# Optimization experiments

Hardware: AMD Instinct MI355X
Metric: run time of the kernel (lower is better)

Reference implementation:

```python
import jax, jax.numpy as jnp
import numpy as np
import math

D_MODEL = 512
N_HEADS = 8
WINDOW = 5
B, S = 4, 2048


def setup_inputs() -> dict:
    key = jax.random.key(0)
    ks = jax.random.split(key, 16)
    d = D_MODEL

    def lin(k, fan_in, fan_out):
        bound = 1.0 / math.sqrt(fan_in)
        kw, kb = jax.random.split(k)
        W = jax.random.uniform(kw, (fan_in, fan_out), jnp.float32, -bound, bound)
        b = jax.random.uniform(kb, (fan_out,), jnp.float32, -bound, bound)
        return W, b

    x = jax.random.normal(ks[0], (B, S, d), jnp.float32)
    W1, b1 = lin(ks[1], d, 2 * d)      # mapping layer 1
    W2, b2 = lin(ks[2], 2 * d, d)      # mapping layer 2
    Wq, bq = lin(ks[3], d, d)
    Wk, bk = lin(ks[4], d, d)
    Wv, bv = lin(ks[5], d, d)
    Wo, bo = lin(ks[6], d, d)
    return dict(x=x, W1=W1, b1=b1, W2=W2, b2=b2, Wq=Wq, bq=bq,
                Wk=Wk, bk=bk, Wv=Wv, bv=bv, Wo=Wo, bo=bo)


def reference(x, W1, b1, W2, b2, Wq, bq, Wk, bk, Wv, bv, Wo, bo):
    Bsz, S_, d = x.shape
    h = N_HEADS
    hd = d // h

    # mapping MLP: Linear -> ReLU -> Linear
    xm = jax.nn.relu(x @ W1 + b1) @ W2 + b2

    def split_heads(t):  # [B,S,d] -> [B,h,S,hd]
        return t.reshape(Bsz, S_, h, hd).transpose(0, 2, 1, 3)

    Q = split_heads(xm @ Wq + bq)
    K = split_heads(xm @ Wk + bk)
    V = split_heads(xm @ Wv + bv)

    scores = jnp.einsum('bhqd,bhkd->bhqk', Q, K) / math.sqrt(hd)

    # inverse sliding-window mask: positions with |i-j| <= window are EXCLUDED
    idx = jnp.arange(S_)
    adjacent = jnp.abs(idx[:, None] - idx[None, :]) <= WINDOW  # [S,S] bool
    scores = jnp.where(adjacent[None, None], -1e9, scores)

    attn = jax.nn.softmax(scores, axis=-1)
    out = jnp.einsum('bhqk,bhkd->bhqd', attn, V)
    out = out.transpose(0, 2, 1, 3).reshape(Bsz, S_, d)
    return out @ Wo + bo
```

## Files before the change

### kernel.cpp

```cpp
#include <hip/hip_runtime.h>
#include <stdint.h>

typedef __attribute__((ext_vector_type(8))) short bf16x8;
typedef __attribute__((ext_vector_type(4))) float f32x4;

__device__ __forceinline__ float bf2f(uint16_t u) {
    union { uint32_t u; float f; } c; c.u = ((uint32_t)u) << 16; return c.f;
}
__device__ __forceinline__ uint16_t f2bf(float f) {
    union { float f; uint32_t u; } c; c.f = f;
    uint32_t r = c.u + 0x7fffu + ((c.u >> 16) & 1u);
    return (uint16_t)(r >> 16);
}
__device__ __forceinline__ uint32_t pk2bf(float a, float b) {
#if __has_builtin(__builtin_amdgcn_cvt_pk_bf16_f32)
    auto v = __builtin_amdgcn_cvt_pk_bf16_f32(a, b);
    uint32_t u; __builtin_memcpy(&u, &v, 4); return u;
#else
    return (uint32_t)f2bf(a) | ((uint32_t)f2bf(b) << 16);
#endif
}
__device__ __forceinline__ float fexp2(float x) {
#if __has_builtin(__builtin_amdgcn_exp2f)
    return __builtin_amdgcn_exp2f(x);
#else
    return exp2f(x);
#endif
}

__device__ __forceinline__ void gld_lds16(const uint16_t* g, uint16_t* l) {
    __builtin_amdgcn_global_load_lds(
        (const __attribute__((address_space(1))) void*)g,
        (__attribute__((address_space(3))) void*)l, 16, 0, 0);
}

__global__ void prep_all(const float* __restrict__ x,
                         const float* __restrict__ W1, const float* __restrict__ W2,
                         const float* __restrict__ Wq, const float* __restrict__ Wk,
                         const float* __restrict__ Wv, const float* __restrict__ Wo,
                         const float* __restrict__ b1, const float* __restrict__ b2,
                         const float* __restrict__ bq, const float* __restrict__ bk,
                         const float* __restrict__ bv, const float* __restrict__ bo,
                         uint16_t* __restrict__ W1T, uint16_t* __restrict__ W2T,
                         uint16_t* __restrict__ WqkvT, uint16_t* __restrict__ WoT,
                         uint16_t* __restrict__ xb, uint16_t* __restrict__ bbase)
{
    const int id = blockIdx.x;
    const int tx = threadIdx.x, ty = threadIdx.y;
    const int tid = ty * 32 + tx;
    if (id < 2048) {
        __shared__ uint16_t t[32][33];
        const float* src; uint16_t* dst; int R, C, tile;
        if      (id < 512)  { src = W1; dst = W1T;              R = 512;  C = 1024; tile = id; }
        else if (id < 1024) { src = W2; dst = W2T;              R = 1024; C = 512;  tile = id - 512; }
        else if (id < 1280) { src = Wq; dst = WqkvT;            R = 512;  C = 512;  tile = id - 1024; }
        else if (id < 1536) { src = Wk; dst = WqkvT + 512*512;  R = 512;  C = 512;  tile = id - 1280; }
        else if (id < 1792) { src = Wv; dst = WqkvT + 1024*512; R = 512;  C = 512;  tile = id - 1536; }
        else                { src = Wo; dst = WoT;              R = 512;  C = 512;  tile = id - 1792; }
        const int ntx = C / 32;
        const int bx = (tile % ntx) * 32, by = (tile / ntx) * 32;
#pragma unroll
        for (int i = ty; i < 32; i += 8) t[i][tx] = f2bf(src[(size_t)(by + i) * C + bx + tx]);
        __syncthreads();
#pragma unroll
        for (int i = ty; i < 32; i += 8) dst[(size_t)(bx + i) * R + by + tx] = t[tx][i];
    } else if (id < 6144) {
        int i = (id - 2048) * 256 + tid;
        float4 v = ((const float4*)x)[i];
        ushort4 o;
        o.x = f2bf(v.x); o.y = f2bf(v.y); o.z = f2bf(v.z); o.w = f2bf(v.w);
        ((ushort4*)xb)[i] = o;
    } else {
        int i = (id - 6144) * 256 + tid;
        if      (i < 1024) bbase[i] = f2bf(b1[i]);
        else if (i < 1536) bbase[i] = f2bf(b2[i - 1024]);
        else if (i < 2048) bbase[i] = f2bf(bq[i - 1536]);
        else if (i < 2560) bbase[i] = f2bf(bk[i - 2048]);
        else if (i < 3072) bbase[i] = f2bf(bv[i - 2560]);
        else if (i < 3584) bbase[i] = f2bf(bo[i - 3072]);
    }
}

template<int RELU, int F32OUT>
__global__ __launch_bounds__(256)
void gemm_k(const uint16_t* __restrict__ A, const uint16_t* __restrict__ Bt,
            const uint16_t* __restrict__ bias, void* __restrict__ Cv,
            int M, int N, int K)
{
    __shared__ __align__(16) uint16_t lsA[128 * 64];
    __shared__ __align__(16) uint16_t lsB[128 * 64];

    const int tid = threadIdx.x, lane = tid & 63;
    const int wid = tid >> 6;
    const int quad = lane >> 4, lm = lane & 15;
    const int wm = wid >> 1, wn = wid & 1;
    const int m0 = blockIdx.y * 128, n0 = blockIdx.x * 128;

    f32x4 acc[4][4];
#pragma unroll
    for (int i = 0; i < 4; ++i)
#pragma unroll
        for (int j = 0; j < 4; ++j) acc[i][j] = (f32x4){0.f, 0.f, 0.f, 0.f};

    for (int k0 = 0; k0 < K; k0 += 64) {
        __syncthreads();
#pragma unroll
        for (int c4 = 0; c4 < 4; ++c4) {
            const int chunk = c4 * 256 + tid;
            const int r = chunk >> 3, lc = (chunk & 7) ^ (r & 7);
            gld_lds16(A  + (size_t)(m0 + r) * K + k0 + lc * 8, lsA + (size_t)chunk * 8);
            gld_lds16(Bt + (size_t)(n0 + r) * K + k0 + lc * 8, lsB + (size_t)chunk * 8);
        }
        __syncthreads();

#pragma unroll
        for (int kh = 0; kh < 2; ++kh) {
            bf16x8 af[4], bfr[4];
#pragma unroll
            for (int t = 0; t < 4; ++t) {
                const int pcA = ((kh * 4 + quad) ^ (lm & 7));
                af[t]  = *(const bf16x8*)(lsA + (wm * 64 + t * 16 + lm) * 64 + pcA * 8);
                bfr[t] = *(const bf16x8*)(lsB + (wn * 64 + t * 16 + lm) * 64 + pcA * 8);
            }
#pragma unroll
            for (int i = 0; i < 4; ++i)
#pragma unroll
                for (int j = 0; j < 4; ++j)
                    acc[i][j] = __builtin_amdgcn_mfma_f32_16x16x32_bf16(af[i], bfr[j], acc[i][j], 0, 0, 0);
        }
    }

#pragma unroll
    for (int i = 0; i < 4; ++i) {
        const int r0 = m0 + wm * 64 + i * 16 + quad * 4;
#pragma unroll
        for (int j = 0; j < 4; ++j) {
            const int col = n0 + wn * 64 + j * 16 + lm;
            const float bvj = bf2f(bias[col]);
#pragma unroll
            for (int r = 0; r < 4; ++r) {
                float v = acc[i][j][r] + bvj;
                if (RELU) v = fmaxf(v, 0.f);
                if (F32OUT) ((float*)Cv)[(size_t)(r0 + r) * N + col] = v;
                else        ((uint16_t*)Cv)[(size_t)(r0 + r) * N + col] = f2bf(v);
            }
        }
    }
}

template<int RELU, int F32OUT>
__global__ __launch_bounds__(256)
void gemm_k64(const uint16_t* __restrict__ A, const uint16_t* __restrict__ Bt,
              const uint16_t* __restrict__ bias, void* __restrict__ Cv,
              int M, int N, int K)
{
    __shared__ __align__(16) uint16_t lsA[64 * 64];
    __shared__ __align__(16) uint16_t lsB[128 * 64];

    const int tid = threadIdx.x, lane = tid & 63;
    const int wid = tid >> 6;
    const int quad = lane >> 4, lm = lane & 15;
    const int wm = wid >> 1, wn = wid & 1;
    const int m0 = blockIdx.y * 64, n0 = blockIdx.x * 128;

    f32x4 acc[2][4];
#pragma unroll
    for (int i = 0; i < 2; ++i)
#pragma unroll
        for (int j = 0; j < 4; ++j) acc[i][j] = (f32x4){0.f, 0.f, 0.f, 0.f};

    for (int k0 = 0; k0 < K; k0 += 64) {
        __syncthreads();
#pragma unroll
        for (int c4 = 0; c4 < 2; ++c4) {
            const int chunk = c4 * 256 + tid;
            const int r = chunk >> 3, lc = (chunk & 7) ^ (r & 7);
            gld_lds16(A + (size_t)(m0 + r) * K + k0 + lc * 8, lsA + (size_t)chunk * 8);
        }
#pragma unroll
        for (int c4 = 0; c4 < 4; ++c4) {
            const int chunk = c4 * 256 + tid;
            const int r = chunk >> 3, lc = (chunk & 7) ^ (r & 7);
            gld_lds16(Bt + (size_t)(n0 + r) * K + k0 + lc * 8, lsB + (size_t)chunk * 8);
        }
        __syncthreads();

#pragma unroll
        for (int kh = 0; kh < 2; ++kh) {
            const int pc = ((kh * 4 + quad) ^ (lm & 7));
            bf16x8 af[2], bfr[4];
#pragma unroll
            for (int t = 0; t < 2; ++t)
                af[t] = *(const bf16x8*)(lsA + (wm * 32 + t * 16 + lm) * 64 + pc * 8);
#pragma unroll
            for (int t = 0; t < 4; ++t)
                bfr[t] = *(const bf16x8*)(lsB + (wn * 64 + t * 16 + lm) * 64 + pc * 8);
#pragma unroll
            for (int i = 0; i < 2; ++i)
#pragma unroll
                for (int j = 0; j < 4; ++j)
                    acc[i][j] = __builtin_amdgcn_mfma_f32_16x16x32_bf16(af[i], bfr[j], acc[i][j], 0, 0, 0);
        }
    }

#pragma unroll
    for (int i = 0; i < 2; ++i) {
        const int r0 = m0 + wm * 32 + i * 16 + quad * 4;
#pragma unroll
        for (int j = 0; j < 4; ++j) {
            const int col = n0 + wn * 64 + j * 16 + lm;
            const float bvj = bf2f(bias[col]);
#pragma unroll
            for (int r = 0; r < 4; ++r) {
                float v = acc[i][j][r] + bvj;
                if (RELU) v = fmaxf(v, 0.f);
                if (F32OUT) ((float*)Cv)[(size_t)(r0 + r) * N + col] = v;
                else        ((uint16_t*)Cv)[(size_t)(r0 + r) * N + col] = f2bf(v);
            }
        }
    }
}

__global__ __launch_bounds__(256)
void gemm_qkv_s(const uint16_t* __restrict__ A, const uint16_t* __restrict__ Bt,
                const uint16_t* __restrict__ bq, const uint16_t* __restrict__ bk,
                const uint16_t* __restrict__ bv_,
                uint16_t* __restrict__ qk, uint16_t* __restrict__ Vt)
{
    __shared__ __align__(16) uint16_t lsA[128 * 64];
    __shared__ __align__(16) uint16_t lsB[128 * 64];

    const int tid = threadIdx.x, lane = tid & 63;
    const int wid = tid >> 6;
    const int quad = lane >> 4, lm = lane & 15;
    const int wm = wid >> 1, wn = wid & 1;
    const int m0 = blockIdx.y * 128, n0 = blockIdx.x * 128;
    const int part = n0 >> 9;
    const uint16_t* B = (part == 0) ? bq : (part == 1) ? bk : bv_;
    const int K = 512;

    f32x4 acc[4][4];
#pragma unroll
    for (int i = 0; i < 4; ++i)
#pragma unroll
        for (int j = 0; j < 4; ++j) acc[i][j] = (f32x4){0.f, 0.f, 0.f, 0.f};

    for (int k0 = 0; k0 < K; k0 += 64) {
        __syncthreads();
#pragma unroll
        for (int c4 = 0; c4 < 4; ++c4) {
            const int chunk = c4 * 256 + tid;
            const int r = chunk >> 3, lc = (chunk & 7) ^ (r & 7);
            gld_lds16(A  + (size_t)(m0 + r) * K + k0 + lc * 8, lsA + (size_t)chunk * 8);
            gld_lds16(Bt + (size_t)(n0 + r) * K + k0 + lc * 8, lsB + (size_t)chunk * 8);
        }
        __syncthreads();

#pragma unroll
        for (int kh = 0; kh < 2; ++kh) {
            const int pc = ((kh * 4 + quad) ^ (lm & 7));
            bf16x8 af[4], bfr[4];
#pragma unroll
            for (int t = 0; t < 4; ++t) {
                af[t]  = *(const bf16x8*)(lsA + (wm * 64 + t * 16 + lm) * 64 + pc * 8);
                bfr[t] = *(const bf16x8*)(lsB + (wn * 64 + t * 16 + lm) * 64 + pc * 8);
            }
#pragma unroll
            for (int i = 0; i < 4; ++i)
#pragma unroll
                for (int j = 0; j < 4; ++j)
                    acc[i][j] = __builtin_amdgcn_mfma_f32_16x16x32_bf16(af[i], bfr[j], acc[i][j], 0, 0, 0);
        }
    }

#pragma unroll
    for (int i = 0; i < 4; ++i) {
        const int mb = m0 + wm * 64 + i * 16 + quad * 4;
#pragma unroll
        for (int j = 0; j < 4; ++j) {
            const int nl = (n0 & 511) + wn * 64 + j * 16 + lm;
            const float bvj = bf2f(B[nl]);
            if (part < 2) {
#pragma unroll
                for (int r = 0; r < 4; ++r)
                    qk[(size_t)(mb + r) * 1024 + part * 512 + nl] = f2bf(acc[i][j][r] + bvj);
            } else {
                const int h = nl >> 6, d = nl & 63;
                const int b = mb >> 11, s0 = mb & 2047;
                const int sp = (s0 & ~31) | ((s0 & 12) << 1) | (((s0 >> 4) & 1) << 2);
                const size_t base = ((size_t)(((b << 3) | h)) * 64 + d) * 2048 + sp;
#pragma unroll
                for (int r = 0; r < 4; ++r)
                    Vt[base + r] = f2bf(acc[i][j][r] + bvj);
            }
        }
    }
}

__global__ __launch_bounds__(256, 2)
void attn_k(const uint16_t* __restrict__ qk, const uint16_t* __restrict__ Vt,
            uint16_t* __restrict__ Out)
{
    __shared__ __align__(16) uint16_t lsK[2][128 * 64];
    __shared__ __align__(16) uint16_t lsV[2][64 * 128];

    const int tid = threadIdx.x, lane = tid & 63, wid = tid >> 6;
    const int quad = lane >> 4, lm = lane & 15;
    const int bh = blockIdx.y, b = bh >> 3, h = bh & 7;
    const int q0 = blockIdx.x * 128;
    const float cscale = 0.125f * 1.44269504088896f;

    bf16x8 qf[2][2];
#pragma unroll
    for (int i = 0; i < 2; ++i)
#pragma unroll
        for (int ks = 0; ks < 2; ++ks) {
            bf16x8 q = *(const bf16x8*)(qk +
                (size_t)(b * 2048 + q0 + wid * 32 + i * 16 + lm) * 1024 + h * 64 + ks * 32 + quad * 8);
#pragma unroll
            for (int e = 0; e < 8; ++e)
                q[e] = (short)f2bf(bf2f((uint16_t)q[e]) * cscale);
            qf[i][ks] = q;
        }

    f32x4 oacc[2][4];
#pragma unroll
    for (int i = 0; i < 2; ++i)
#pragma unroll
        for (int n = 0; n < 4; ++n) oacc[i][n] = (f32x4){0.f, 0.f, 0.f, 0.f};
    float lrow[2] = {0.f, 0.f};

    auto stage = [&](int j0, int bb) {
#pragma unroll
        for (int c4 = 0; c4 < 4; ++c4) {
            const int chunk = c4 * 256 + tid;
            const int r = chunk >> 3, lc = (chunk & 7) ^ (r & 7);
            gld_lds16(qk + (size_t)(b * 2048 + j0 + r) * 1024 + 512 + h * 64 + lc * 8,
                      &lsK[bb][(size_t)chunk * 8]);
        }
#pragma unroll
        for (int c4 = 0; c4 < 4; ++c4) {
            const int chunk = c4 * 256 + tid;
            const int d = chunk >> 4, lc = (chunk & 15) ^ (d & 15);
            gld_lds16(Vt + (size_t)(bh * 64 + d) * 2048 + j0 + lc * 8,
                      &lsV[bb][(size_t)chunk * 8]);
        }
    };

    auto compute = [&](int j0, int bb) {
        const uint16_t* Kb = &lsK[bb][0];
        const uint16_t* Vb = &lsV[bb][0];

        f32x4 sacc[2][8];
#pragma unroll
        for (int i = 0; i < 2; ++i)
#pragma unroll
            for (int j = 0; j < 8; ++j) sacc[i][j] = (f32x4){0.f, 0.f, 0.f, 0.f};
        __builtin_amdgcn_s_setprio(1);
#pragma unroll
        for (int ks = 0; ks < 2; ++ks)
#pragma unroll
            for (int j = 0; j < 8; ++j) {
                const int pc = (ks * 4 + quad) ^ (lm & 7);
                bf16x8 kf = *(const bf16x8*)(Kb + (j * 16 + lm) * 64 + pc * 8);
#pragma unroll
                for (int i = 0; i < 2; ++i)
                    sacc[i][j] = __builtin_amdgcn_mfma_f32_16x16x32_bf16(kf, qf[i][ks], sacc[i][j], 0, 0, 0);
            }
        __builtin_amdgcn_s_setprio(0);

        if ((j0 + 127 >= q0 - 5) && (j0 <= q0 + 127 + 5)) {
#pragma unroll
            for (int i = 0; i < 2; ++i) {
                const int qr = q0 + wid * 32 + i * 16 + lm;
#pragma unroll
                for (int j = 0; j < 8; ++j)
#pragma unroll
                    for (int r = 0; r < 4; ++r) {
                        int kc = j0 + j * 16 + quad * 4 + r;
                        int dd = qr - kc; if (dd < 0) dd = -dd;
                        if (dd <= 5) sacc[i][j][r] = -1e30f;
                    }
            }
        }

#pragma unroll
        for (int ks = 0; ks < 4; ++ks) {
            bf16x8 pa[2];
#pragma unroll
            for (int i = 0; i < 2; ++i) {
                const float p0 = fexp2(sacc[i][2 * ks + 0][0]);
                const float p1 = fexp2(sacc[i][2 * ks + 0][1]);
                const float p2 = fexp2(sacc[i][2 * ks + 0][2]);
                const float p3 = fexp2(sacc[i][2 * ks + 0][3]);
                const float p4 = fexp2(sacc[i][2 * ks + 1][0]);
                const float p5 = fexp2(sacc[i][2 * ks + 1][1]);
                const float p6 = fexp2(sacc[i][2 * ks + 1][2]);
                const float p7 = fexp2(sacc[i][2 * ks + 1][3]);
                lrow[i] += ((p0 + p1) + (p2 + p3)) + ((p4 + p5) + (p6 + p7));
                union { bf16x8 v; uint32_t u[4]; } c;
                c.u[0] = pk2bf(p0, p1);
                c.u[1] = pk2bf(p2, p3);
                c.u[2] = pk2bf(p4, p5);
                c.u[3] = pk2bf(p6, p7);
                pa[i] = c.v;
            }
            __builtin_amdgcn_s_setprio(1);
#pragma unroll
            for (int n = 0; n < 4; ++n) {
                const int pc = (ks * 4 + quad) ^ lm;
                bf16x8 vf = *(const bf16x8*)(Vb + (n * 16 + lm) * 128 + pc * 8);
#pragma unroll
                for (int i = 0; i < 2; ++i)
                    oacc[i][n] = __builtin_amdgcn_mfma_f32_16x16x32_bf16(pa[i], vf, oacc[i][n], 0, 0, 0);
            }
            __builtin_amdgcn_s_setprio(0);
        }
    };

    stage(0, 0);
    int cur = 0;
#pragma unroll 1
    for (int jt = 0; jt < 15; ++jt) {
        stage((jt + 1) * 128, cur ^ 1);
        asm volatile("s_waitcnt vmcnt(8)" ::: "memory");
        __builtin_amdgcn_sched_barrier(0);
        __builtin_amdgcn_s_barrier();
        compute(jt * 128, cur);
        __builtin_amdgcn_s_barrier();
        cur ^= 1;
    }
    asm volatile("s_waitcnt vmcnt(0)" ::: "memory");
    __builtin_amdgcn_sched_barrier(0);
    __builtin_amdgcn_s_barrier();
    compute(15 * 128, cur);

#pragma unroll
    for (int i = 0; i < 2; ++i) {
        float l = lrow[i];
        l += __shfl_xor(l, 16);
        l += __shfl_xor(l, 32);
        const float inv = 1.f / (l + 1e-30f);
#pragma unroll
        for (int r = 0; r < 4; ++r) {
            const float invr = __shfl(inv, quad * 4 + r, 16);
            const int s = q0 + wid * 32 + i * 16 + quad * 4 + r;
#pragma unroll
            for (int n = 0; n < 4; ++n)
                Out[(size_t)(b * 2048 + s) * 512 + h * 64 + n * 16 + lm] = f2bf(oacc[i][n][r] * invr);
        }
    }
}

extern "C" void kernel_launch(void* const* d_in, const int* in_sizes, int n_in,
                              void* d_out, int out_size, void* d_ws, size_t ws_size,
                              hipStream_t stream)
{
    const float* x  = (const float*)d_in[0];
    const float* W1 = (const float*)d_in[1];
    const float* b1 = (const float*)d_in[2];
    const float* W2 = (const float*)d_in[3];
    const float* b2 = (const float*)d_in[4];
    const float* Wq = (const float*)d_in[5];
    const float* bq = (const float*)d_in[6];
    const float* Wk = (const float*)d_in[7];
    const float* bk = (const float*)d_in[8];
    const float* Wv = (const float*)d_in[9];
    const float* bv = (const float*)d_in[10];
    const float* Wo = (const float*)d_in[11];
    const float* bo = (const float*)d_in[12];
    (void)in_sizes; (void)n_in; (void)out_size; (void)ws_size;

    char* ws = (char*)d_ws;
    const size_t MiB = 1024 * 1024;
    uint16_t* xb    = (uint16_t*)(ws + 0);
    uint16_t* W1T   = (uint16_t*)(ws + 8 * MiB);
    uint16_t* W2T   = (uint16_t*)(ws + 9 * MiB);
    uint16_t* WqkvT = (uint16_t*)(ws + 10 * MiB);
    uint16_t* WoT   = (uint16_t*)(ws + 11 * MiB + 512 * 1024);
    uint16_t* bbase = (uint16_t*)(ws + 12 * MiB);
    uint16_t* b1b = bbase, *b2b = bbase + 1024, *bqb = bbase + 1536;
    uint16_t* bkb = bbase + 2048, *bvb = bbase + 2560, *bob = bbase + 3072;
    uint16_t* xm1   = (uint16_t*)(ws + 13 * MiB);
    uint16_t* xm    = (uint16_t*)(ws + 29 * MiB);
    uint16_t* qk    = xm1;
    uint16_t* att   = xm;
    uint16_t* Vt    = xb;

    prep_all<<<6158, dim3(32, 8), 0, stream>>>(x, W1, W2, Wq, Wk, Wv, Wo,
                                               b1, b2, bq, bk, bv, bo,
                                               W1T, W2T, WqkvT, WoT, xb, bbase);

    gemm_k<1,0>  <<<dim3(8, 64),  256, 0, stream>>>(xb,  W1T, b1b, xm1, 8192, 1024, 512);
    gemm_k64<0,0><<<dim3(4, 128), 256, 0, stream>>>(xm1, W2T, b2b, xm,  8192, 512, 1024);
    gemm_qkv_s   <<<dim3(12, 64), 256, 0, stream>>>(xm, WqkvT, bqb, bkb, bvb, qk, Vt);
    attn_k       <<<dim3(16, 32), 256, 0, stream>>>(qk, Vt, att);
    gemm_k64<0,1><<<dim3(4, 128), 256, 0, stream>>>(att, WoT, bob, d_out, 8192, 512, 512);
}
```

Measured before the change: 217.2 us.

## Split attention key tile across two wave groups with LDS reduction

Doubles the attention block to 512 threads. Two groups of four waves each handle half of every 128-key tile for the same 128 queries. Their partial PV accumulators and row sums are then combined through LDS before normalisation. The aim is more waves in flight and fewer registers per wave, to hide latency in the attention loop. The cost is an extra LDS reduction, extra barriers, and duplicated Q fragment loads.

```diff
diff --git a/kernel.cpp b/kernel.cpp
--- a/kernel.cpp
+++ b/kernel.cpp
@@ -297,14 +297,14 @@
     }
 }
 
-__global__ __launch_bounds__(256, 2)
+__global__ __launch_bounds__(512, 4)
 void attn_k(const uint16_t* __restrict__ qk, const uint16_t* __restrict__ Vt,
             uint16_t* __restrict__ Out)
 {
-    __shared__ __align__(16) uint16_t lsK[2][128 * 64];
-    __shared__ __align__(16) uint16_t lsV[2][64 * 128];
+    __shared__ __align__(16) uint16_t lsAll[2][16384];
 
     const int tid = threadIdx.x, lane = tid & 63, wid = tid >> 6;
+    const int qw = wid & 3, kh2 = wid >> 2;
     const int quad = lane >> 4, lm = lane & 15;
     const int bh = blockIdx.y, b = bh >> 3, h = bh & 7;
     const int q0 = blockIdx.x * 128;
@@ -316,7 +316,7 @@
 #pragma unroll
         for (int ks = 0; ks < 2; ++ks) {
             bf16x8 q = *(const bf16x8*)(qk +
-                (size_t)(b * 2048 + q0 + wid * 32 + i * 16 + lm) * 1024 + h * 64 + ks * 32 + quad * 8);
+                (size_t)(b * 2048 + q0 + qw * 32 + i * 16 + lm) * 1024 + h * 64 + ks * 32 + quad * 8);
 #pragma unroll
             for (int e = 0; e < 8; ++e)
                 q[e] = (short)f2bf(bf2f((uint16_t)q[e]) * cscale);
@@ -331,38 +331,40 @@
     float lrow[2] = {0.f, 0.f};
 
     auto stage = [&](int j0, int bb) {
-#pragma unroll
-        for (int c4 = 0; c4 < 4; ++c4) {
-            const int chunk = c4 * 256 + tid;
+        uint16_t* lsK = &lsAll[bb][0];
+        uint16_t* lsV = &lsAll[bb][8192];
+#pragma unroll
+        for (int c2 = 0; c2 < 2; ++c2) {
+            const int chunk = c2 * 512 + tid;
             const int r = chunk >> 3, lc = (chunk & 7) ^ (r & 7);
             gld_lds16(qk + (size_t)(b * 2048 + j0 + r) * 1024 + 512 + h * 64 + lc * 8,
-                      &lsK[bb][(size_t)chunk * 8]);
-        }
-#pragma unroll
-        for (int c4 = 0; c4 < 4; ++c4) {
-            const int chunk = c4 * 256 + tid;
+                      lsK + (size_t)chunk * 8);
+        }
+#pragma unroll
+        for (int c2 = 0; c2 < 2; ++c2) {
+            const int chunk = c2 * 512 + tid;
             const int d = chunk >> 4, lc = (chunk & 15) ^ (d & 15);
             gld_lds16(Vt + (size_t)(bh * 64 + d) * 2048 + j0 + lc * 8,
-                      &lsV[bb][(size_t)chunk * 8]);
+                      lsV + (size_t)chunk * 8);
         }
     };
 
     auto compute = [&](int j0, int bb) {
-        const uint16_t* Kb = &lsK[bb][0];
-        const uint16_t* Vb = &lsV[bb][0];
-
-        f32x4 sacc[2][8];
+        const uint16_t* Kb = &lsAll[bb][0];
+        const uint16_t* Vb = &lsAll[bb][8192];
+
+        f32x4 sacc[2][4];
 #pragma unroll
         for (int i = 0; i < 2; ++i)
 #pragma unroll
-            for (int j = 0; j < 8; ++j) sacc[i][j] = (f32x4){0.f, 0.f, 0.f, 0.f};
+            for (int j = 0; j < 4; ++j) sacc[i][j] = (f32x4){0.f, 0.f, 0.f, 0.f};
         __builtin_amdgcn_s_setprio(1);
 #pragma unroll
         for (int ks = 0; ks < 2; ++ks)
 #pragma unroll
-            for (int j = 0; j < 8; ++j) {
+            for (int j = 0; j < 4; ++j) {
                 const int pc = (ks * 4 + quad) ^ (lm & 7);
-                bf16x8 kf = *(const bf16x8*)(Kb + (j * 16 + lm) * 64 + pc * 8);
+                bf16x8 kf = *(const bf16x8*)(Kb + (kh2 * 64 + j * 16 + lm) * 64 + pc * 8);
 #pragma unroll
                 for (int i = 0; i < 2; ++i)
                     sacc[i][j] = __builtin_amdgcn_mfma_f32_16x16x32_bf16(kf, qf[i][ks], sacc[i][j], 0, 0, 0);
@@ -372,12 +374,12 @@
         if ((j0 + 127 >= q0 - 5) && (j0 <= q0 + 127 + 5)) {
 #pragma unroll
             for (int i = 0; i < 2; ++i) {
-                const int qr = q0 + wid * 32 + i * 16 + lm;
-#pragma unroll
-                for (int j = 0; j < 8; ++j)
+                const int qr = q0 + qw * 32 + i * 16 + lm;
+#pragma unroll
+                for (int j = 0; j < 4; ++j)
 #pragma unroll
                     for (int r = 0; r < 4; ++r) {
-                        int kc = j0 + j * 16 + quad * 4 + r;
+                        int kc = j0 + kh2 * 64 + j * 16 + quad * 4 + r;
                         int dd = qr - kc; if (dd < 0) dd = -dd;
                         if (dd <= 5) sacc[i][j][r] = -1e30f;
                     }
@@ -385,18 +387,19 @@
         }
 
 #pragma unroll
-        for (int ks = 0; ks < 4; ++ks) {
+        for (int ksl = 0; ksl < 2; ++ksl) {
+            const int gs = kh2 * 2 + ksl;
             bf16x8 pa[2];
 #pragma unroll
             for (int i = 0; i < 2; ++i) {
-                const float p0 = fexp2(sacc[i][2 * ks + 0][0]);
-                const float p1 = fexp2(sacc[i][2 * ks + 0][1]);
-                const float p2 = fexp2(sacc[i][2 * ks + 0][2]);
-                const float p3 = fexp2(sacc[i][2 * ks + 0][3]);
-                const float p4 = fexp2(sacc[i][2 * ks + 1][0]);
-                const float p5 = fexp2(sacc[i][2 * ks + 1][1]);
-                const float p6 = fexp2(sacc[i][2 * ks + 1][2]);
-                const float p7 = fexp2(sacc[i][2 * ks + 1][3]);
+                const float p0 = fexp2(sacc[i][2 * ksl + 0][0]);
+                const float p1 = fexp2(sacc[i][2 * ksl + 0][1]);
+                const float p2 = fexp2(sacc[i][2 * ksl + 0][2]);
+                const float p3 = fexp2(sacc[i][2 * ksl + 0][3]);
+                const float p4 = fexp2(sacc[i][2 * ksl + 1][0]);
+                const float p5 = fexp2(sacc[i][2 * ksl + 1][1]);
+                const float p6 = fexp2(sacc[i][2 * ksl + 1][2]);
+                const float p7 = fexp2(sacc[i][2 * ksl + 1][3]);
                 lrow[i] += ((p0 + p1) + (p2 + p3)) + ((p4 + p5) + (p6 + p7));
                 union { bf16x8 v; uint32_t u[4]; } c;
                 c.u[0] = pk2bf(p0, p1);
@@ -408,7 +411,7 @@
             __builtin_amdgcn_s_setprio(1);
 #pragma unroll
             for (int n = 0; n < 4; ++n) {
-                const int pc = (ks * 4 + quad) ^ lm;
+                const int pc = (gs * 4 + quad) ^ lm;
                 bf16x8 vf = *(const bf16x8*)(Vb + (n * 16 + lm) * 128 + pc * 8);
 #pragma unroll
                 for (int i = 0; i < 2; ++i)
@@ -423,7 +426,7 @@
 #pragma unroll 1
     for (int jt = 0; jt < 15; ++jt) {
         stage((jt + 1) * 128, cur ^ 1);
-        asm volatile("s_waitcnt vmcnt(8)" ::: "memory");
+        asm volatile("s_waitcnt vmcnt(4)" ::: "memory");
         __builtin_amdgcn_sched_barrier(0);
         __builtin_amdgcn_s_barrier();
         compute(jt * 128, cur);
@@ -435,19 +438,40 @@
     __builtin_amdgcn_s_barrier();
     compute(15 * 128, cur);
 
-#pragma unroll
-    for (int i = 0; i < 2; ++i) {
-        float l = lrow[i];
-        l += __shfl_xor(l, 16);
-        l += __shfl_xor(l, 32);
-        const float inv = 1.f / (l + 1e-30f);
-#pragma unroll
-        for (int r = 0; r < 4; ++r) {
-            const float invr = __shfl(inv, quad * 4 + r, 16);
-            const int s = q0 + wid * 32 + i * 16 + quad * 4 + r;
-#pragma unroll
-            for (int n = 0; n < 4; ++n)
-                Out[(size_t)(b * 2048 + s) * 512 + h * 64 + n * 16 + lm] = f2bf(oacc[i][n][r] * invr);
+    __syncthreads();
+    f32x4* red = (f32x4*)&lsAll[0][0];
+    if (wid >= 4) {
+        const int base = ((wid - 4) * 64 + lane) * 9;
+#pragma unroll
+        for (int i = 0; i < 2; ++i)
+#pragma unroll
+            for (int n = 0; n < 4; ++n) red[base + i * 4 + n] = oacc[i][n];
+        red[base + 8] = (f32x4){lrow[0], lrow[1], 0.f, 0.f};
+    }
+    __syncthreads();
+    if (wid < 4) {
+        const int base = (wid * 64 + lane) * 9;
+#pragma unroll
+        for (int i = 0; i < 2; ++i)
+#pragma unroll
+            for (int n = 0; n < 4; ++n) oacc[i][n] += red[base + i * 4 + n];
+        const f32x4 lr = red[base + 8];
+        lrow[0] += lr[0]; lrow[1] += lr[1];
+
+#pragma unroll
+        for (int i = 0; i < 2; ++i) {
+            float l = lrow[i];
+            l += __shfl_xor(l, 16);
+            l += __shfl_xor(l, 32);
+            const float inv = 1.f / (l + 1e-30f);
+#pragma unroll
+            for (int r = 0; r < 4; ++r) {
+                const float invr = __shfl(inv, quad * 4 + r, 16);
+                const int s = q0 + wid * 32 + i * 16 + quad * 4 + r;
+#pragma unroll
+                for (int n = 0; n < 4; ++n)
+                    Out[(size_t)(b * 2048 + s) * 512 + h * 64 + n * 16 + lm] = f2bf(oacc[i][n][r] * invr);
+            }
         }
     }
 }
@@ -494,6 +518,6 @@
     gemm_k<1,0>  <<<dim3(8, 64),  256, 0, stream>>>(xb,  W1T, b1b, xm1, 8192, 1024, 512);
     gemm_k64<0,0><<<dim3(4, 128), 256, 0, stream>>>(xm1, W2T, b2b, xm,  8192, 512, 1024);
     gemm_qkv_s   <<<dim3(12, 64), 256, 0, stream>>>(xm, WqkvT, bqb, bkb, bvb, qk, Vt);
-    attn_k       <<<dim3(16, 32), 256, 0, stream>>>(qk, Vt, att);
+    attn_k       <<<dim3(16, 32), 512, 0, stream>>>(qk, Vt, att);
     gemm_k64<0,1><<<dim3(4, 128), 256, 0, stream>>>(att, WoT, bob, d_out, 8192, 512, 512);
 }
```

New measurement: 214.1 us. No clear change (-1.4%).
